# Kernel optimization log

Measured on AMD Instinct MI355X. Metric: run time of the kernel, lower is better.

## Reference

```python
import jax, jax.numpy as jnp
import numpy as np

EPS = 1e-06

def _quantize_weights(W):
    # absmean ternary quantization: sign(W/gamma) * clamp(round(|W/gamma|), max=1)
    gamma = jnp.mean(jnp.abs(W)) + EPS
    Ws = W / gamma
    return jnp.sign(Ws) * jnp.minimum(jnp.round(jnp.abs(Ws)), 1.0)

def setup_inputs() -> dict:
    key = jax.random.key(0)
    kx, kw = jax.random.split(key)
    x = jax.random.normal(kx, (4, 2048, 4096), dtype=jnp.float32)
    weight = jax.random.normal(kw, (16384, 4096), dtype=jnp.float32)
    return {"x": x, "weight": weight}

def reference(x, weight):
    xs = jnp.sign(x)                       # binarized activations in {-1,0,1}
    Wq = _quantize_weights(weight)          # ternary weights in {-1,0,1}
    # F.linear(x, W) == x @ W.T ; [b, s, in] x [out, in] -> [b, s, out]
    return jnp.einsum('bsi,oi->bso', xs, Wq)
```

## Files before the change

kernel.cpp:

```cpp
#include <hip/hip_runtime.h>
#include <hip/hip_bf16.h>
#include <cstdint>

constexpr int Mx = 8192;
constexpr int Kx = 4096;
constexpr int Nx = 16384;
constexpr long W_ELEMS = (long)Nx * Kx;
constexpr long X_ELEMS = (long)Mx * Kx;
constexpr int KB = Kx / 2;

typedef int v4i __attribute__((ext_vector_type(4)));
typedef int v8i __attribute__((ext_vector_type(8)));
typedef float v16f __attribute__((ext_vector_type(16)));

#define GLOBAL_AS(p) ((const __attribute__((address_space(1))) void*)(p))
#define LDS_AS(p)    ((__attribute__((address_space(3))) void*)(p))

template <int P> struct IC { static constexpr int value = P; };

__global__ __launch_bounds__(256) void absum_kernel(const float4* __restrict__ W4,
                                                    double* __restrict__ partials) {
    int t = threadIdx.x;
    long base = (long)blockIdx.x * 8192;
    double s = 0.0;
#pragma unroll 4
    for (int i = 0; i < 32; ++i) {
        float4 v = W4[base + (long)i * 256 + t];
        s += (double)fabsf(v.x) + (double)fabsf(v.y) +
             (double)fabsf(v.z) + (double)fabsf(v.w);
    }
    __shared__ double sm[256];
    sm[t] = s;
    __syncthreads();
    for (int off = 128; off > 0; off >>= 1) {
        if (t < off) sm[t] += sm[t + off];
        __syncthreads();
    }
    if (t == 0) partials[blockIdx.x] = sm[0];
}

__global__ __launch_bounds__(256) void finalize_kernel(const double* __restrict__ partials,
                                                       float* __restrict__ thr) {
    int t = threadIdx.x;
    double s = 0.0;
#pragma unroll
    for (int i = 0; i < 8; ++i) s += partials[(long)i * 256 + t];
    __shared__ double sm[256];
    sm[t] = s;
    __syncthreads();
    for (int off = 128; off > 0; off >>= 1) {
        if (t < off) sm[t] += sm[t + off];
        __syncthreads();
    }
    if (t == 0) {
        double gamma = sm[0] / (double)W_ELEMS + 1e-6;
        *thr = (float)(0.5 * gamma);
    }
}

__device__ __forceinline__ uint32_t enc_t(float v, float thr) {
    return (fabsf(v) > thr) ? ((v > 0.f) ? 0x2u : 0xAu) : 0x0u;
}

__device__ __forceinline__ uint32_t pack8(float4 a, float4 b, float thr) {
    return enc_t(a.x, thr)        | (enc_t(a.y, thr) << 4)  |
          (enc_t(a.z, thr) << 8)  | (enc_t(a.w, thr) << 12) |
          (enc_t(b.x, thr) << 16) | (enc_t(b.y, thr) << 20) |
          (enc_t(b.z, thr) << 24) | (enc_t(b.w, thr) << 28);
}

__global__ __launch_bounds__(256) void quantw_kernel(const float4* __restrict__ W4,
                                                     uint4* __restrict__ out,
                                                     const float* __restrict__ thrp) {
    float thr = *thrp;
    long gt = (long)blockIdx.x * 256 + threadIdx.x;
    uint32_t d0 = pack8(W4[gt * 8 + 0], W4[gt * 8 + 1], thr);
    uint32_t d1 = pack8(W4[gt * 8 + 2], W4[gt * 8 + 3], thr);
    uint32_t d2 = pack8(W4[gt * 8 + 4], W4[gt * 8 + 5], thr);
    uint32_t d3 = pack8(W4[gt * 8 + 6], W4[gt * 8 + 7], thr);
    out[gt] = make_uint4(d0, d1, d2, d3);
}

__global__ __launch_bounds__(256) void quantx_kernel(const float4* __restrict__ X4,
                                                     uint4* __restrict__ out) {
    long gt = (long)blockIdx.x * 256 + threadIdx.x;
    uint32_t d0 = pack8(X4[gt * 8 + 0], X4[gt * 8 + 1], 0.f);
    uint32_t d1 = pack8(X4[gt * 8 + 2], X4[gt * 8 + 3], 0.f);
    uint32_t d2 = pack8(X4[gt * 8 + 4], X4[gt * 8 + 5], 0.f);
    uint32_t d3 = pack8(X4[gt * 8 + 6], X4[gt * 8 + 7], 0.f);
    out[gt] = make_uint4(d0, d1, d2, d3);
}

__global__ __launch_bounds__(512) void gemm_fp4(const uint8_t* __restrict__ A,
                                                const uint8_t* __restrict__ B,
                                                float* __restrict__ C) {
    __shared__ __align__(16) uint8_t smem[8 * 16384];

    const int t = threadIdx.x;
    const int l = t & 63;
    const int wid = t >> 6;
    const int wm = wid >> 2;
    const int wn = wid & 3;
    const int lr = l & 31;
    const int lh = l >> 5;

    int wg = blockIdx.x;
    int sw = (wg & 7) * 256 + (wg >> 3);
    int bm = sw & 31;
    int bn = sw >> 5;
    const long m0 = (long)bm * 256;
    const long n0 = (long)bn * 256;

    const int r0s = t >> 2;
    const int cb0 = (((t & 3) ^ ((r0s >> 1) & 3)) << 4);
    const int voff0 = r0s * KB + cb0;
    const int voff1 = voff0 + 128 * KB;
    const uint8_t* Abase = A + m0 * (long)KB;
    const uint8_t* Bbase = B + n0 * (long)KB;
    const int lo0 = t * 16, lo1 = t * 16 + 8192;

    auto swz = [](int r, int c) {
        return r * 64 + ((c ^ ((r >> 1) & 3)) << 4);
    };
    int offA[2][4], offB[2][2];
#pragma unroll
    for (int h = 0; h < 2; ++h) {
#pragma unroll
        for (int mt = 0; mt < 4; ++mt)
            offA[h][mt] = swz(wm * 128 + mt * 32 + lr, h * 2 + lh);
#pragma unroll
        for (int nt = 0; nt < 2; ++nt)
            offB[h][nt] = swz(wn * 64 + nt * 32 + lr, h * 2 + lh);
    }

    v16f acc[4][2] = {};

#pragma unroll
    for (int j = 0; j < 5; ++j) {
        int tj = j >> 1, slot = j;
        const uint8_t* s = (j & 1) ? Bbase : Abase;
        __builtin_amdgcn_global_load_lds(GLOBAL_AS(s + tj * 64 + voff0), LDS_AS(smem + slot * 16384 + lo0), 16, 0, 0);
        __builtin_amdgcn_global_load_lds(GLOBAL_AS(s + tj * 64 + voff1), LDS_AS(smem + slot * 16384 + lo1), 16, 0, 0);
    }
    asm volatile("s_waitcnt vmcnt(6)" ::: "memory");
    asm volatile("s_barrier" ::: "memory");

#pragma unroll 2
    for (int tau = 0; tau < 32; ++tau) {
        auto phase = [&](auto hc) {
            constexpr int h = decltype(hc)::value;
            const int sA = (2 * tau) & 7;
            const int sB = sA + 1;
            v8i ar8[4], br8[2];
#pragma unroll
            for (int mt = 0; mt < 4; ++mt) {
                v4i v = *(const v4i*)(smem + sA * 16384 + offA[h][mt]);
                ar8[mt] = __builtin_shufflevector(v, v, 0, 1, 2, 3, -1, -1, -1, -1);
            }
#pragma unroll
            for (int nt = 0; nt < 2; ++nt) {
                v4i v = *(const v4i*)(smem + sB * 16384 + offB[h][nt]);
                br8[nt] = __builtin_shufflevector(v, v, 0, 1, 2, 3, -1, -1, -1, -1);
            }
            {
                int j = 2 * tau + h + 5;
                if (j < 64) {
                    int tj = j >> 1, slot = j & 7;
                    const uint8_t* s = (j & 1) ? Bbase : Abase;
                    __builtin_amdgcn_global_load_lds(GLOBAL_AS(s + tj * 64 + voff0), LDS_AS(smem + slot * 16384 + lo0), 16, 0, 0);
                    __builtin_amdgcn_global_load_lds(GLOBAL_AS(s + tj * 64 + voff1), LDS_AS(smem + slot * 16384 + lo1), 16, 0, 0);
                }
            }
            __builtin_amdgcn_s_setprio(1);
#pragma unroll
            for (int mt = 0; mt < 4; ++mt)
#pragma unroll
                for (int nt = 0; nt < 2; ++nt)
                    acc[mt][nt] = __builtin_amdgcn_mfma_scale_f32_32x32x64_f8f6f4(
                        ar8[mt], br8[nt], acc[mt][nt], 4, 4, 0, 0x7F7F7F7F, 0, 0x7F7F7F7F);
            __builtin_amdgcn_s_setprio(0);
            if constexpr (h == 1) {
                if (tau <= 28)      asm volatile("s_waitcnt vmcnt(6)" ::: "memory");
                else if (tau == 29) asm volatile("s_waitcnt vmcnt(4)" ::: "memory");
                else if (tau == 30) asm volatile("s_waitcnt vmcnt(0)" ::: "memory");
            }
            asm volatile("s_barrier" ::: "memory");
        };
        phase(IC<0>{});
        phase(IC<1>{});
    }

#pragma unroll
    for (int mt = 0; mt < 4; ++mt) {
        long rbase = m0 + wm * 128 + mt * 32 + 4 * lh;
#pragma unroll
        for (int nt = 0; nt < 2; ++nt) {
            long gcol = n0 + wn * 64 + nt * 32 + lr;
#pragma unroll
            for (int r = 0; r < 16; ++r) {
                long grow = rbase + (r & 3) + 8 * (r >> 2);
                C[grow * Nx + gcol] = acc[mt][nt][r];
            }
        }
    }
}

extern "C" void kernel_launch(void* const* d_in, const int* in_sizes, int n_in,
                              void* d_out, int out_size, void* d_ws, size_t ws_size,
                              hipStream_t stream) {
    const float* x = (const float*)d_in[0];
    const float* weight = (const float*)d_in[1];
    float* out = (float*)d_out;

    uint8_t* xq = (uint8_t*)d_ws;
    uint8_t* wq = xq + X_ELEMS / 2;
    double* partials = (double*)((char*)d_ws + X_ELEMS / 2 + W_ELEMS / 2);
    float* thr = (float*)((char*)d_ws + X_ELEMS / 2 + W_ELEMS / 2 + 2048 * sizeof(double));

    absum_kernel<<<2048, 256, 0, stream>>>((const float4*)weight, partials);
    finalize_kernel<<<1, 256, 0, stream>>>(partials, thr);
    quantw_kernel<<<8192, 256, 0, stream>>>((const float4*)weight, (uint4*)wq, thr);
    quantx_kernel<<<4096, 256, 0, stream>>>((const float4*)x, (uint4*)xq);
    gemm_fp4<<<2048, 512, 0, stream>>>(xq, wq, out);
}
```

Measured before the change: 571.2 us.

## Use 1024-thread GEMM blocks with 16 waves each owning a 64x64 tile

The FP4 GEMM block grows from 8 to 16 waves while keeping the 256x256 block tile. Each wave now computes a 64x64 sub-tile with 4 MFMA accumulators instead of 128x64 with 8. Each thread issues one global-to-LDS load per stage instead of two, and the vmcnt waits are adjusted to match. This is meant to add latency hiding and spread staging work across more waves, at the cost of more LDS fragment reads per MFMA and more waves contending at each barrier.

```diff
diff --git a/kernel.cpp b/kernel.cpp
--- a/kernel.cpp
+++ b/kernel.cpp
@@ -91,9 +91,9 @@
     out[gt] = make_uint4(d0, d1, d2, d3);
 }
 
-__global__ __launch_bounds__(512) void gemm_fp4(const uint8_t* __restrict__ A,
-                                                const uint8_t* __restrict__ B,
-                                                float* __restrict__ C) {
+__global__ __launch_bounds__(1024) void gemm_fp4(const uint8_t* __restrict__ A,
+                                                 const uint8_t* __restrict__ B,
+                                                 float* __restrict__ C) {
     __shared__ __align__(16) uint8_t smem[8 * 16384];
 
     const int t = threadIdx.x;
@@ -113,36 +113,34 @@
 
     const int r0s = t >> 2;
     const int cb0 = (((t & 3) ^ ((r0s >> 1) & 3)) << 4);
-    const int voff0 = r0s * KB + cb0;
-    const int voff1 = voff0 + 128 * KB;
+    const int voff = r0s * KB + cb0;
     const uint8_t* Abase = A + m0 * (long)KB;
     const uint8_t* Bbase = B + n0 * (long)KB;
-    const int lo0 = t * 16, lo1 = t * 16 + 8192;
+    const int lo = t * 16;
 
     auto swz = [](int r, int c) {
         return r * 64 + ((c ^ ((r >> 1) & 3)) << 4);
     };
-    int offA[2][4], offB[2][2];
+    int offA[2][2], offB[2][2];
 #pragma unroll
     for (int h = 0; h < 2; ++h) {
 #pragma unroll
-        for (int mt = 0; mt < 4; ++mt)
-            offA[h][mt] = swz(wm * 128 + mt * 32 + lr, h * 2 + lh);
+        for (int mt = 0; mt < 2; ++mt)
+            offA[h][mt] = swz(wm * 64 + mt * 32 + lr, h * 2 + lh);
 #pragma unroll
         for (int nt = 0; nt < 2; ++nt)
             offB[h][nt] = swz(wn * 64 + nt * 32 + lr, h * 2 + lh);
     }
 
-    v16f acc[4][2] = {};
+    v16f acc[2][2] = {};
 
 #pragma unroll
     for (int j = 0; j < 5; ++j) {
-        int tj = j >> 1, slot = j;
         const uint8_t* s = (j & 1) ? Bbase : Abase;
-        __builtin_amdgcn_global_load_lds(GLOBAL_AS(s + tj * 64 + voff0), LDS_AS(smem + slot * 16384 + lo0), 16, 0, 0);
-        __builtin_amdgcn_global_load_lds(GLOBAL_AS(s + tj * 64 + voff1), LDS_AS(smem + slot * 16384 + lo1), 16, 0, 0);
-    }
-    asm volatile("s_waitcnt vmcnt(6)" ::: "memory");
+        __builtin_amdgcn_global_load_lds(GLOBAL_AS(s + (j >> 1) * 64 + voff),
+                                         LDS_AS(smem + j * 16384 + lo), 16, 0, 0);
+    }
+    asm volatile("s_waitcnt vmcnt(3)" ::: "memory");
     asm volatile("s_barrier" ::: "memory");
 
 #pragma unroll 2
@@ -151,37 +149,44 @@
             constexpr int h = decltype(hc)::value;
             const int sA = (2 * tau) & 7;
             const int sB = sA + 1;
-            v8i ar8[4], br8[2];
-#pragma unroll
-            for (int mt = 0; mt < 4; ++mt) {
-                v4i v = *(const v4i*)(smem + sA * 16384 + offA[h][mt]);
-                ar8[mt] = __builtin_shufflevector(v, v, 0, 1, 2, 3, -1, -1, -1, -1);
-            }
-#pragma unroll
-            for (int nt = 0; nt < 2; ++nt) {
-                v4i v = *(const v4i*)(smem + sB * 16384 + offB[h][nt]);
-                br8[nt] = __builtin_shufflevector(v, v, 0, 1, 2, 3, -1, -1, -1, -1);
+            v8i a0, a1, b0, b1;
+            {
+                v4i v = *(const v4i*)(smem + sA * 16384 + offA[h][0]);
+                a0 = __builtin_shufflevector(v, v, 0, 1, 2, 3, -1, -1, -1, -1);
+            }
+            {
+                v4i v = *(const v4i*)(smem + sA * 16384 + offA[h][1]);
+                a1 = __builtin_shufflevector(v, v, 0, 1, 2, 3, -1, -1, -1, -1);
+            }
+            {
+                v4i v = *(const v4i*)(smem + sB * 16384 + offB[h][0]);
+                b0 = __builtin_shufflevector(v, v, 0, 1, 2, 3, -1, -1, -1, -1);
+            }
+            {
+                v4i v = *(const v4i*)(smem + sB * 16384 + offB[h][1]);
+                b1 = __builtin_shufflevector(v, v, 0, 1, 2, 3, -1, -1, -1, -1);
             }
             {
                 int j = 2 * tau + h + 5;
                 if (j < 64) {
-                    int tj = j >> 1, slot = j & 7;
                     const uint8_t* s = (j & 1) ? Bbase : Abase;
-                    __builtin_amdgcn_global_load_lds(GLOBAL_AS(s + tj * 64 + voff0), LDS_AS(smem + slot * 16384 + lo0), 16, 0, 0);
-                    __builtin_amdgcn_global_load_lds(GLOBAL_AS(s + tj * 64 + voff1), LDS_AS(smem + slot * 16384 + lo1), 16, 0, 0);
+                    __builtin_amdgcn_global_load_lds(GLOBAL_AS(s + (j >> 1) * 64 + voff),
+                                                     LDS_AS(smem + (j & 7) * 16384 + lo), 16, 0, 0);
                 }
             }
             __builtin_amdgcn_s_setprio(1);
-#pragma unroll
-            for (int mt = 0; mt < 4; ++mt)
-#pragma unroll
-                for (int nt = 0; nt < 2; ++nt)
-                    acc[mt][nt] = __builtin_amdgcn_mfma_scale_f32_32x32x64_f8f6f4(
-                        ar8[mt], br8[nt], acc[mt][nt], 4, 4, 0, 0x7F7F7F7F, 0, 0x7F7F7F7F);
+            acc[0][0] = __builtin_amdgcn_mfma_scale_f32_32x32x64_f8f6f4(
+                a0, b0, acc[0][0], 4, 4, 0, 0x7F7F7F7F, 0, 0x7F7F7F7F);
+            acc[0][1] = __builtin_amdgcn_mfma_scale_f32_32x32x64_f8f6f4(
+                a0, b1, acc[0][1], 4, 4, 0, 0x7F7F7F7F, 0, 0x7F7F7F7F);
+            acc[1][0] = __builtin_amdgcn_mfma_scale_f32_32x32x64_f8f6f4(
+                a1, b0, acc[1][0], 4, 4, 0, 0x7F7F7F7F, 0, 0x7F7F7F7F);
+            acc[1][1] = __builtin_amdgcn_mfma_scale_f32_32x32x64_f8f6f4(
+                a1, b1, acc[1][1], 4, 4, 0, 0x7F7F7F7F, 0, 0x7F7F7F7F);
             __builtin_amdgcn_s_setprio(0);
             if constexpr (h == 1) {
-                if (tau <= 28)      asm volatile("s_waitcnt vmcnt(6)" ::: "memory");
-                else if (tau == 29) asm volatile("s_waitcnt vmcnt(4)" ::: "memory");
+                if (tau <= 28)      asm volatile("s_waitcnt vmcnt(3)" ::: "memory");
+                else if (tau == 29) asm volatile("s_waitcnt vmcnt(2)" ::: "memory");
                 else if (tau == 30) asm volatile("s_waitcnt vmcnt(0)" ::: "memory");
             }
             asm volatile("s_barrier" ::: "memory");
@@ -191,8 +196,8 @@
     }
 
 #pragma unroll
-    for (int mt = 0; mt < 4; ++mt) {
-        long rbase = m0 + wm * 128 + mt * 32 + 4 * lh;
+    for (int mt = 0; mt < 2; ++mt) {
+        long rbase = m0 + wm * 64 + mt * 32 + 4 * lh;
 #pragma unroll
         for (int nt = 0; nt < 2; ++nt) {
             long gcol = n0 + wn * 64 + nt * 32 + lr;
@@ -221,5 +226,5 @@
     finalize_kernel<<<1, 256, 0, stream>>>(partials, thr);
     quantw_kernel<<<8192, 256, 0, stream>>>((const float4*)weight, (uint4*)wq, thr);
     quantx_kernel<<<4096, 256, 0, stream>>>((const float4*)x, (uint4*)xq);
-    gemm_fp4<<<2048, 512, 0, stream>>>(xq, wq, out);
-}
+    gemm_fp4<<<2048, 1024, 0, stream>>>(xq, wq, out);
+}
```

Result: slower. 1.050 ms (+83.8%).
